# Performance work log

Measured on AMD Instinct MI355X. Metric: run time of the kernel, lower is better.

## Reference

```python
import jax, jax.numpy as jnp
import numpy as np

BITS = 4
MASK = (1 << BITS) - 1  # 15


def _dequant(qweight, scales, qzeros, groupsize):
    # qweight: [in//32*bits, out] int32; 8 nibbles packed per int32 along rows.
    out_f = qweight.shape[1]
    shifts = jnp.arange(0, 32, BITS, dtype=jnp.int32)  # [8]
    # [rows, 8, out] -> unpacked int weights in [0, 15]
    w = (qweight[:, None, :] >> shifts[None, :, None]) & MASK
    w = w.reshape(-1, groupsize, out_f)  # [n_groups, groupsize, out]
    s = scales.reshape(-1, 1, out_f)     # [n_groups, 1, out]
    z = qzeros.reshape(-1, 1, out_f)
    W = s * w.astype(scales.dtype) - z * s
    return W.reshape(-1, out_f)          # [in, out]


def setup_inputs() -> dict:
    key = jax.random.key(0)
    k1, k2, k3, k4, k5 = jax.random.split(key, 5)
    B, S, IN, OUT, G = 4, 2048, 4096, 4096, 64
    x = jax.random.normal(k1, (B, S, IN), dtype=jnp.float16)
    qweight = jax.random.randint(k2, (IN // 32 * BITS, OUT), 0, 2147483647, dtype=jnp.int32)
    scales = (jax.random.uniform(k3, (IN // G, OUT), dtype=jnp.float32) * 0.01 + 0.001).astype(jnp.float16)
    qzeros = (jax.random.uniform(k4, (IN // G, OUT), dtype=jnp.float32) * 15.0).astype(jnp.float16)
    bias = jax.random.normal(k5, (OUT,), dtype=jnp.float16)
    return {"x": x, "qweight": qweight, "scales": scales, "qzeros": qzeros,
            "bias": bias, "groupsize": G, "bits": BITS}


def reference(x, qweight, scales, qzeros, bias, groupsize, bits):
    W = _dequant(qweight, scales, qzeros, groupsize)  # [in, out] fp16
    return jnp.matmul(x, W) + bias
```

## Files before the change

### kernel.cpp

```cpp
#include <hip/hip_runtime.h>
#include <stdint.h>
#include <stddef.h>

typedef __bf16 bf16;
typedef __bf16 bf16x8 __attribute__((ext_vector_type(8)));
typedef float  f32x4  __attribute__((ext_vector_type(4)));

#define GLOBAL_AS(p) ((const __attribute__((address_space(1))) void*)(p))
#define LDS_AS(p)    ((__attribute__((address_space(3))) void*)(p))

__device__ __forceinline__ void gload_lds16(const bf16* g, bf16* l) {
    __builtin_amdgcn_global_load_lds(GLOBAL_AS(g), LDS_AS(l), 16, 0, 0);
}

__global__ __launch_bounds__(256)
void convert_x_kernel(const float* __restrict__ x, bf16* __restrict__ xb, long n8) {
    long t = (long)blockIdx.x * blockDim.x + threadIdx.x;
    if (t >= n8) return;
    const f32x4* p = (const f32x4*)(x + t * 8);
    f32x4 a = p[0], b = p[1];
    bf16x8 v;
#pragma unroll
    for (int j = 0; j < 4; ++j) { v[j] = (bf16)a[j]; v[4 + j] = (bf16)b[j]; }
    *(bf16x8*)(xb + t * 8) = v;
}

__global__ __launch_bounds__(256)
void dequant_wt_kernel(const uint32_t* __restrict__ qw,
                       const float* __restrict__ scales,
                       const float* __restrict__ qzeros,
                       bf16* __restrict__ Wt,
                       int N, int K, int rows_per_group) {
    int rows = K >> 3;
    int t = blockIdx.x * blockDim.x + threadIdx.x;
    int o = t / rows;
    int r = t - o * rows;
    if (o >= N) return;
    uint32_t q = qw[(size_t)r * N + o];
    int g = r / rows_per_group;
    float s = scales[(size_t)g * N + o];
    float z = qzeros[(size_t)g * N + o];
    float nsz = -s * z;
    bf16x8 v;
#pragma unroll
    for (int j = 0; j < 8; ++j)
        v[j] = (bf16)fmaf((float)((q >> (4 * j)) & 15u), s, nsz);
    *(bf16x8*)(Wt + (size_t)o * K + (size_t)r * 8) = v;
}

constexpr int BM = 128, BN = 128, BK = 32;

template <bool FUSED>
__global__ __launch_bounds__(256)
void gemm_kernel(const bf16* __restrict__ Ab,
                 const float* __restrict__ Af,
                 const bf16* __restrict__ Bt,
                 const uint32_t* __restrict__ qw,
                 const float* __restrict__ scales,
                 const float* __restrict__ qzeros,
                 const float* __restrict__ bias,
                 float* __restrict__ out,
                 int M, int N, int K, int G) {
    __shared__ __align__(16) bf16 As[BM * BK];
    __shared__ __align__(16) bf16 Bs[BN * BK];

    const int tid  = threadIdx.x;
    const int lane = tid & 63;
    const int wave = tid >> 6;
    const int wm = wave & 1;
    const int wn = wave >> 1;
    const int m0 = blockIdx.y * BM;
    const int n0 = blockIdx.x * BN;

    const int lrow = lane & 15;
    const int lk8  = (lane >> 4) * 8;

    f32x4 acc[4][4];
#pragma unroll
    for (int i = 0; i < 4; ++i)
#pragma unroll
        for (int j = 0; j < 4; ++j) acc[i][j] = (f32x4){0.f, 0.f, 0.f, 0.f};

    for (int kt = 0; kt < K; kt += BK) {
        if (!FUSED) {
#pragma unroll
            for (int it = 0; it < 2; ++it) {
                const int c = tid + it * 256;
                const int row = c >> 2;
                const int kc  = (c & 3) * 8;
                gload_lds16(Ab + (size_t)(m0 + row) * K + kt + kc, As + c * 8);
                gload_lds16(Bt + (size_t)(n0 + row) * K + kt + kc, Bs + c * 8);
            }
        } else {
#pragma unroll
            for (int it = 0; it < 2; ++it) {
                const int c = tid + it * 256;
                const int row = c >> 2;
                const int kc  = (c & 3) * 8;
                const f32x4* p = (const f32x4*)(Af + (size_t)(m0 + row) * K + kt + kc);
                f32x4 a = p[0], b = p[1];
                bf16x8 v;
#pragma unroll
                for (int j = 0; j < 4; ++j) { v[j] = (bf16)a[j]; v[4 + j] = (bf16)b[j]; }
                *(bf16x8*)(As + row * BK + kc) = v;
            }
            const int g = kt / G;
#pragma unroll
            for (int it = 0; it < 2; ++it) {
                const int idx = tid + it * 256;
                const int rl = idx >> 7;
                const int nl = idx & 127;
                uint32_t q = qw[(size_t)(kt / 8 + rl) * N + n0 + nl];
                float s = scales[(size_t)g * N + n0 + nl];
                float z = qzeros[(size_t)g * N + n0 + nl];
                float nsz = -s * z;
                bf16x8 v;
#pragma unroll
                for (int j = 0; j < 8; ++j)
                    v[j] = (bf16)fmaf((float)((q >> (4 * j)) & 15u), s, nsz);
                *(bf16x8*)(Bs + nl * BK + rl * 8) = v;
            }
        }
        __syncthreads();

        bf16x8 a[4], b[4];
#pragma unroll
        for (int i = 0; i < 4; ++i)
            a[i] = *(const bf16x8*)(As + (wm * 64 + i * 16 + lrow) * BK + lk8);
#pragma unroll
        for (int j = 0; j < 4; ++j)
            b[j] = *(const bf16x8*)(Bs + (wn * 64 + j * 16 + lrow) * BK + lk8);

#pragma unroll
        for (int i = 0; i < 4; ++i)
#pragma unroll
            for (int j = 0; j < 4; ++j)
                acc[i][j] = __builtin_amdgcn_mfma_f32_16x16x32_bf16(
                    a[i], b[j], acc[i][j], 0, 0, 0);
        __syncthreads();
    }

#pragma unroll
    for (int j = 0; j < 4; ++j) {
        const int col = n0 + wn * 64 + j * 16 + (lane & 15);
        const float bv = bias[col];
#pragma unroll
        for (int i = 0; i < 4; ++i) {
            const int rbase = m0 + wm * 64 + i * 16 + (lane >> 4) * 4;
#pragma unroll
            for (int r = 0; r < 4; ++r)
                out[(size_t)(rbase + r) * N + col] = acc[i][j][r] + bv;
        }
    }
}

extern "C" void kernel_launch(void* const* d_in, const int* in_sizes, int n_in,
                              void* d_out, int out_size, void* d_ws, size_t ws_size,
                              hipStream_t stream) {
    const float*    x      = (const float*)d_in[0];
    const uint32_t* qw     = (const uint32_t*)d_in[1];
    const float*    scales = (const float*)d_in[2];
    const float*    qzeros = (const float*)d_in[3];
    const float*    bias   = (const float*)d_in[4];
    float*          out    = (float*)d_out;

    const int N = in_sizes[4];
    const int K = (in_sizes[1] / N) * 8;
    const int M = in_sizes[0] / K;
    const int G = K / (in_sizes[2] / N);

    dim3 grid(N / BN, M / BM);
    const size_t xb_bytes = (size_t)M * K * sizeof(bf16);
    const size_t wt_bytes = (size_t)N * K * sizeof(bf16);

    if (ws_size >= xb_bytes + wt_bytes) {
        bf16* Xb = (bf16*)d_ws;
        bf16* Wt = (bf16*)((char*)d_ws + xb_bytes);
        const long n8 = (long)M * K / 8;
        convert_x_kernel<<<(int)((n8 + 255) / 256), 256, 0, stream>>>(x, Xb, n8);
        const int total = (K >> 3) * N;
        dequant_wt_kernel<<<(total + 255) / 256, 256, 0, stream>>>(
            qw, scales, qzeros, Wt, N, K, G / 8);
        gemm_kernel<false><<<grid, 256, 0, stream>>>(
            Xb, nullptr, Wt, nullptr, scales, qzeros, bias, out, M, N, K, G);
    } else {
        gemm_kernel<true><<<grid, 256, 0, stream>>>(
            nullptr, x, nullptr, qw, scales, qzeros, bias, out, M, N, K, G);
    }
}
```

Baseline: 586.2 us.

## Store dequantized weights in K-tiled layout for contiguous GEMM B-tile loads

The dequant kernel now writes weights as [K/32][N][32] tiles instead of [N][K], and the GEMM reads each B tile as one contiguous block of memory. This is meant to make the global-to-LDS loads for B fully contiguous and to improve the coalescing of the dequant reads of qweight (16 columns by 4 rows per wave). The cost is a more complex index mapping; the LDS layout and the MFMA path are unchanged.

```diff
diff --git a/kernel.cpp b/kernel.cpp
--- a/kernel.cpp
+++ b/kernel.cpp
@@ -26,26 +26,29 @@
 }
 
 __global__ __launch_bounds__(256)
-void dequant_wt_kernel(const uint32_t* __restrict__ qw,
-                       const float* __restrict__ scales,
-                       const float* __restrict__ qzeros,
-                       bf16* __restrict__ Wt,
-                       int N, int K, int rows_per_group) {
-    int rows = K >> 3;
-    int t = blockIdx.x * blockDim.x + threadIdx.x;
-    int o = t / rows;
-    int r = t - o * rows;
+void dequant_wt_tiled_kernel(const uint32_t* __restrict__ qw,
+                             const float* __restrict__ scales,
+                             const float* __restrict__ qzeros,
+                             bf16* __restrict__ Wt,
+                             int N, int K, int rows_per_group) {
+    const int i = blockIdx.x * 256 + threadIdx.x;
+    const int w = i >> 6, l = i & 63;
+    const int nrq = K >> 5;
+    const int rq = w % nrq;
+    const int o  = (w / nrq) * 16 + (l >> 2);
+    const int c  = l & 3;
+    const int r  = rq * 4 + c;
     if (o >= N) return;
-    uint32_t q = qw[(size_t)r * N + o];
-    int g = r / rows_per_group;
-    float s = scales[(size_t)g * N + o];
-    float z = qzeros[(size_t)g * N + o];
-    float nsz = -s * z;
+    const uint32_t q = qw[(size_t)r * N + o];
+    const int g = r / rows_per_group;
+    const float s = scales[(size_t)g * N + o];
+    const float z = qzeros[(size_t)g * N + o];
+    const float nsz = -s * z;
     bf16x8 v;
 #pragma unroll
     for (int j = 0; j < 8; ++j)
         v[j] = (bf16)fmaf((float)((q >> (4 * j)) & 15u), s, nsz);
-    *(bf16x8*)(Wt + (size_t)o * K + (size_t)r * 8) = v;
+    *(bf16x8*)(Wt + (size_t)rq * N * 32 + (size_t)o * 32 + c * 8) = v;
 }
 
 constexpr int BM = 128, BN = 128, BK = 32;
@@ -83,13 +86,14 @@
 
     for (int kt = 0; kt < K; kt += BK) {
         if (!FUSED) {
+            const bf16* bsrc = Bt + (size_t)(kt >> 5) * N * 32 + (size_t)n0 * 32;
 #pragma unroll
             for (int it = 0; it < 2; ++it) {
                 const int c = tid + it * 256;
                 const int row = c >> 2;
                 const int kc  = (c & 3) * 8;
                 gload_lds16(Ab + (size_t)(m0 + row) * K + kt + kc, As + c * 8);
-                gload_lds16(Bt + (size_t)(n0 + row) * K + kt + kc, Bs + c * 8);
+                gload_lds16(bsrc + c * 8, Bs + c * 8);
             }
         } else {
 #pragma unroll
@@ -178,8 +182,8 @@
         bf16* Wt = (bf16*)((char*)d_ws + xb_bytes);
         const long n8 = (long)M * K / 8;
         convert_x_kernel<<<(int)((n8 + 255) / 256), 256, 0, stream>>>(x, Xb, n8);
-        const int total = (K >> 3) * N;
-        dequant_wt_kernel<<<(total + 255) / 256, 256, 0, stream>>>(
+        const long dq_threads = ((long)N / 16) * (K >> 5) * 64;
+        dequant_wt_tiled_kernel<<<(int)((dq_threads + 255) / 256), 256, 0, stream>>>(
             qw, scales, qzeros, Wt, N, K, G / 8);
         gemm_kernel<false><<<grid, 256, 0, stream>>>(
             Xb, nullptr, Wt, nullptr, scales, qzeros, bias, out, M, N, K, G);
```

Result: faster. 561.7 us (-4.2%).
